# Kernel tuning notes

Hardware: AMD Instinct MI355X
Metric: run time of the kernel (lower is better)

Reference implementation:

```python
import jax, jax.numpy as jnp
import numpy as np

CX = 256  # args.Cx in the original repo (hidden channel dim)

def setup_inputs() -> dict:
    key = jax.random.key(0)
    kK, kV, kQ = jax.random.split(key, 3)
    N, Cx, Tx, Ty = 16, CX, 2048, 2048
    K = jax.random.normal(kK, (N, Cx, Tx), dtype=jnp.float32)
    V = jax.random.normal(kV, (N, Cx, Tx), dtype=jnp.float32)
    Q = jax.random.normal(kQ, (N, Cx, Ty), dtype=jnp.float32)
    return {"K": K, "V": V, "Q": Q}

def reference(K, V, Q):
    # scores: (N, Tx, Ty) = K^T Q / sqrt(Cx)
    scale = 1.0 / np.sqrt(CX).astype(np.float32)
    scores = jnp.einsum('nct,ncy->nty', K, Q) * scale
    A = jax.nn.softmax(scores, axis=1)          # softmax over Tx (dim=1)
    R = jnp.einsum('nct,nty->ncy', V, A)         # (N, Cx, Ty)
    return (R, A)
```

## Files before the change

### kernel.cpp

```cpp
#include <hip/hip_runtime.h>

#define NB 16
#define CX 256
#define TX 2048
#define TY 2048
#define SCALE 0.0625f

typedef __attribute__((ext_vector_type(8))) short short8;
typedef __attribute__((ext_vector_type(4))) short short4v;
typedef __attribute__((ext_vector_type(4))) float floatx4;

__device__ float L_dev[NB * TY];

static __device__ __forceinline__ short f2bf(float x) {
#if defined(__gfx950__)
    __bf16 b = (__bf16)x;
    return __builtin_bit_cast(short, b);
#else
    union { float f; unsigned u; } v; v.f = x;
    unsigned r = v.u + 0x7fff + ((v.u >> 16) & 1);
    return (short)(r >> 16);
#endif
}

__global__ __launch_bounds__(256) void k_prep(const float* __restrict__ K,
                                              const float* __restrict__ Q,
                                              short* __restrict__ KT,
                                              short* __restrict__ QT) {
    __shared__ float Tsh[32][36];
    const int tid = threadIdx.x;
    const int t0  = blockIdx.x * 32;
    const int c0  = blockIdx.y * 32;
    const int isQ = blockIdx.z & 1;
    const int n   = blockIdx.z >> 1;
    const float* src = (isQ ? Q : K) + (size_t)n * CX * TX;
    short*       dst = (isQ ? QT : KT) + (size_t)n * TX * CX;
    const float scale = isQ ? 1.0f : SCALE;

    const int r  = tid >> 3;
    const int q4 = (tid & 7) * 4;
    *(floatx4*)&Tsh[r][q4] =
        *(const floatx4*)(src + (size_t)(c0 + r) * TX + t0 + q4);
    __syncthreads();
    short4v o = { f2bf(Tsh[q4 + 0][r] * scale),
                  f2bf(Tsh[q4 + 1][r] * scale),
                  f2bf(Tsh[q4 + 2][r] * scale),
                  f2bf(Tsh[q4 + 3][r] * scale) };
    *(short4v*)(dst + (size_t)(t0 + r) * CX + c0 + q4) = o;
}

__global__ __launch_bounds__(256) void k_zero() {
    L_dev[blockIdx.x * 256 + threadIdx.x] = 0.f;
}

__global__ __launch_bounds__(256) void k_scores2(const short* __restrict__ KT,
                                                 const short* __restrict__ QT,
                                                 float* __restrict__ S) {
    __shared__ short Ksh[128][40];
    __shared__ short Qsh[128][40];
    __shared__ float Lsh[128];
    const int tid = threadIdx.x;
    const int n  = blockIdx.z;
    const int t0 = blockIdx.y * 128;
    const int y0 = blockIdx.x * 128;

    const short* Ka = KT + ((size_t)n * TX + t0) * CX;
    const short* Qa = QT + ((size_t)n * TY + y0) * CX;

    if (tid < 128) Lsh[tid] = 0.f;

    const int sr = tid >> 1;
    const int sc = (tid & 1) * 16;
    const short* Kp = Ka + (size_t)sr * CX + sc;
    const short* Qp = Qa + (size_t)sr * CX + sc;

    const int lane = tid & 63;
    const int w    = tid >> 6;
    const int wy   = (w >> 1) * 64;
    const int wt   = (w & 1) * 64;
    const int fr   = lane & 15;
    const int fq   = lane >> 4;

    floatx4 acc[4][4];
#pragma unroll
    for (int i = 0; i < 4; ++i)
#pragma unroll
        for (int j = 0; j < 4; ++j) acc[i][j] = (floatx4)0.f;

    short8 ra0 = *(const short8*)(Kp + 0);
    short8 ra1 = *(const short8*)(Kp + 8);
    short8 rb0 = *(const short8*)(Qp + 0);
    short8 rb1 = *(const short8*)(Qp + 8);

    for (int k0 = 0; k0 < CX; k0 += 32) {
        *(short8*)&Ksh[sr][sc]     = ra0;
        *(short8*)&Ksh[sr][sc + 8] = ra1;
        *(short8*)&Qsh[sr][sc]     = rb0;
        *(short8*)&Qsh[sr][sc + 8] = rb1;
        __syncthreads();
        if (k0 + 32 < CX) {
            ra0 = *(const short8*)(Kp + k0 + 32);
            ra1 = *(const short8*)(Kp + k0 + 40);
            rb0 = *(const short8*)(Qp + k0 + 32);
            rb1 = *(const short8*)(Qp + k0 + 40);
        }
        short8 af[4], bv[4];
#pragma unroll
        for (int mt = 0; mt < 4; ++mt)
            af[mt] = *(short8*)&Qsh[wy + mt * 16 + fr][fq * 8];
#pragma unroll
        for (int nt = 0; nt < 4; ++nt)
            bv[nt] = *(short8*)&Ksh[wt + nt * 16 + fr][fq * 8];
#pragma unroll
        for (int mt = 0; mt < 4; ++mt)
#pragma unroll
            for (int nt = 0; nt < 4; ++nt)
                acc[mt][nt] = __builtin_amdgcn_mfma_f32_16x16x32_bf16(
                    af[mt], bv[nt], acc[mt][nt], 0, 0, 0);
        __syncthreads();
    }

    float* Sp = S + (size_t)n * TX * TY;
#pragma unroll
    for (int nt = 0; nt < 4; ++nt) {
        const size_t trow = (size_t)(t0 + wt + nt * 16 + fr) * TY;
#pragma unroll
        for (int mt = 0; mt < 4; ++mt)
            *(floatx4*)&Sp[trow + y0 + wy + mt * 16 + fq * 4] = acc[mt][nt];
    }

#pragma unroll
    for (int mt = 0; mt < 4; ++mt) {
#pragma unroll
        for (int reg = 0; reg < 4; ++reg) {
            float v = 0.f;
#pragma unroll
            for (int nt = 0; nt < 4; ++nt) v += __expf(acc[mt][nt][reg]);
            v += __shfl_xor(v, 1);
            v += __shfl_xor(v, 2);
            v += __shfl_xor(v, 4);
            v += __shfl_xor(v, 8);
            if (fr == 0) atomicAdd(&Lsh[wy + mt * 16 + fq * 4 + reg], v);
        }
    }
    __syncthreads();
    if (tid < 128) atomicAdd(&L_dev[(size_t)n * TY + y0 + tid], Lsh[tid]);
}

__global__ __launch_bounds__(512) void k_pv2(const float* __restrict__ V,
                                             float* __restrict__ SA,
                                             float* __restrict__ R) {
    __shared__ short Vsh[256][40];
    __shared__ short Psh[128][40];
    const int tid = threadIdx.x;
    const int n  = blockIdx.y;
    const int y0 = blockIdx.x * 128;

    const float* Vp = V + (size_t)n * CX * TX;
    float* Ap = SA + (size_t)n * TX * TY + y0;
    float* Rp = R + (size_t)n * CX * TY;

    const int tt = tid & 7;
    const int tc = tid >> 3;
    const int sy = tid & 127;
    const int kh = tid >> 7;

    const float inv = 1.0f / L_dev[(size_t)n * TY + y0 + sy];

    const int lane = tid & 63;
    const int w    = tid >> 6;
    const int wy   = (w & 1) * 64;
    const int wc   = (w >> 1) * 64;
    const int fr   = lane & 15;
    const int fq   = lane >> 4;

    floatx4 acc[4][4];
#pragma unroll
    for (int i = 0; i < 4; ++i)
#pragma unroll
        for (int j = 0; j < 4; ++j) acc[i][j] = (floatx4)0.f;

    for (int k0 = 0; k0 < TX; k0 += 32) {
#pragma unroll
        for (int cc = 0; cc < 4; ++cc) {
            const int c = cc * 64 + tc;
            floatx4 v = *(const floatx4*)(Vp + (size_t)c * TX + k0 + tt * 4);
            short4v sv = {f2bf(v[0]), f2bf(v[1]), f2bf(v[2]), f2bf(v[3])};
            *(short4v*)&Vsh[c][tt * 4] = sv;
        }
#pragma unroll
        for (int g = 0; g < 2; ++g) {
            const int t = k0 + kh * 8 + g * 4;
            float* a0p = Ap + (size_t)(t + 0) * TY + sy;
            float* a1p = Ap + (size_t)(t + 1) * TY + sy;
            float* a2p = Ap + (size_t)(t + 2) * TY + sy;
            float* a3p = Ap + (size_t)(t + 3) * TY + sy;
            float a0 = __expf(*a0p) * inv;
            float a1 = __expf(*a1p) * inv;
            float a2 = __expf(*a2p) * inv;
            float a3 = __expf(*a3p) * inv;
            *a0p = a0; *a1p = a1; *a2p = a2; *a3p = a3;
            short4v pv = {f2bf(a0), f2bf(a1), f2bf(a2), f2bf(a3)};
            *(short4v*)&Psh[sy][kh * 8 + g * 4] = pv;
        }
        __syncthreads();
        short8 af[4], bv[4];
#pragma unroll
        for (int mt = 0; mt < 4; ++mt)
            af[mt] = *(short8*)&Psh[wy + mt * 16 + fr][fq * 8];
#pragma unroll
        for (int nt = 0; nt < 4; ++nt)
            bv[nt] = *(short8*)&Vsh[wc + nt * 16 + fr][fq * 8];
#pragma unroll
        for (int mt = 0; mt < 4; ++mt)
#pragma unroll
            for (int nt = 0; nt < 4; ++nt)
                acc[mt][nt] = __builtin_amdgcn_mfma_f32_16x16x32_bf16(
                    af[mt], bv[nt], acc[mt][nt], 0, 0, 0);
        __syncthreads();
    }

#pragma unroll
    for (int nt = 0; nt < 4; ++nt) {
        const size_t crow = (size_t)(wc + nt * 16 + fr) * TY;
#pragma unroll
        for (int mt = 0; mt < 4; ++mt)
            *(floatx4*)&Rp[crow + y0 + wy + mt * 16 + fq * 4] = acc[mt][nt];
    }
}

extern "C" void kernel_launch(void* const* d_in, const int* in_sizes, int n_in,
                              void* d_out, int out_size, void* d_ws, size_t ws_size,
                              hipStream_t stream) {
    (void)in_sizes; (void)n_in; (void)out_size; (void)d_ws; (void)ws_size;
    const float* K = (const float*)d_in[0];
    const float* V = (const float*)d_in[1];
    const float* Q = (const float*)d_in[2];
    float* R = (float*)d_out;
    float* A = (float*)d_out + (size_t)NB * CX * TY;
    short* KT = (short*)d_out;
    short* QT = KT + (size_t)NB * TX * CX;

    dim3 blk(256);
    k_prep   <<<dim3(TX / 32, CX / 32, NB * 2), blk, 0, stream>>>(K, Q, KT, QT);
    k_zero   <<<dim3(NB * TY / 256), blk, 0, stream>>>();
    k_scores2<<<dim3(TY / 128, TX / 128, NB), blk, 0, stream>>>(KT, QT, A);
    k_pv2    <<<dim3(TY / 128, NB), dim3(512), 0, stream>>>(V, A, R);
}
```

Before: 608.1 us.

## Store exponentials in scores kernel and register-prefetch V and A in PV kernel

The scores kernel now writes exp(score) instead of the raw score, so the PV kernel only multiplies by the inverse row sum instead of recomputing exp. The PV kernel is restructured to 256 threads over 64-column y tiles, which gives twice as many blocks. It also prefetches the next V tile and A values into registers so global loads overlap with the MFMA work. This raises register pressure, and V is re-read and converted once per y tile, so more blocks means more total V traffic.

```diff
diff --git a/kernel.cpp b/kernel.cpp
--- a/kernel.cpp
+++ b/kernel.cpp
@@ -55,7 +55,7 @@
 
 __global__ __launch_bounds__(256) void k_scores2(const short* __restrict__ KT,
                                                  const short* __restrict__ QT,
-                                                 float* __restrict__ S) {
+                                                 float* __restrict__ E) {
     __shared__ short Ksh[128][40];
     __shared__ short Qsh[128][40];
     __shared__ float Lsh[128];
@@ -120,13 +120,18 @@
         __syncthreads();
     }
 
-    float* Sp = S + (size_t)n * TX * TY;
+    float* Ep = E + (size_t)n * TX * TY;
 #pragma unroll
     for (int nt = 0; nt < 4; ++nt) {
         const size_t trow = (size_t)(t0 + wt + nt * 16 + fr) * TY;
 #pragma unroll
-        for (int mt = 0; mt < 4; ++mt)
-            *(floatx4*)&Sp[trow + y0 + wy + mt * 16 + fq * 4] = acc[mt][nt];
+        for (int mt = 0; mt < 4; ++mt) {
+            floatx4 e;
+#pragma unroll
+            for (int c = 0; c < 4; ++c) e[c] = __expf(acc[mt][nt][c]);
+            acc[mt][nt] = e;
+            *(floatx4*)&Ep[trow + y0 + wy + mt * 16 + fq * 4] = e;
+        }
     }
 
 #pragma unroll
@@ -135,7 +140,7 @@
         for (int reg = 0; reg < 4; ++reg) {
             float v = 0.f;
 #pragma unroll
-            for (int nt = 0; nt < 4; ++nt) v += __expf(acc[mt][nt][reg]);
+            for (int nt = 0; nt < 4; ++nt) v += acc[mt][nt][reg];
             v += __shfl_xor(v, 1);
             v += __shfl_xor(v, 2);
             v += __shfl_xor(v, 4);
@@ -147,30 +152,29 @@
     if (tid < 128) atomicAdd(&L_dev[(size_t)n * TY + y0 + tid], Lsh[tid]);
 }
 
-__global__ __launch_bounds__(512) void k_pv2(const float* __restrict__ V,
-                                             float* __restrict__ SA,
+__global__ __launch_bounds__(256) void k_pv3(const float* __restrict__ V,
+                                             float* __restrict__ EA,
                                              float* __restrict__ R) {
     __shared__ short Vsh[256][40];
-    __shared__ short Psh[128][40];
+    __shared__ short Psh[64][40];
     const int tid = threadIdx.x;
     const int n  = blockIdx.y;
-    const int y0 = blockIdx.x * 128;
+    const int y0 = blockIdx.x * 64;
 
     const float* Vp = V + (size_t)n * CX * TX;
-    float* Ap = SA + (size_t)n * TX * TY + y0;
+    float* Ap = EA + (size_t)n * TX * TY + y0;
     float* Rp = R + (size_t)n * CX * TY;
 
     const int tt = tid & 7;
     const int tc = tid >> 3;
-    const int sy = tid & 127;
-    const int kh = tid >> 7;
+    const int sy = tid & 63;
+    const int kh = tid >> 6;
 
     const float inv = 1.0f / L_dev[(size_t)n * TY + y0 + sy];
 
     const int lane = tid & 63;
     const int w    = tid >> 6;
-    const int wy   = (w & 1) * 64;
-    const int wc   = (w >> 1) * 64;
+    const int wc   = w * 64;
     const int fr   = lane & 15;
     const int fq   = lane >> 4;
 
@@ -180,34 +184,46 @@
 #pragma unroll
         for (int j = 0; j < 4; ++j) acc[i][j] = (floatx4)0.f;
 
+    floatx4 rv[8];
+    float   ra[8];
+#pragma unroll
+    for (int cc = 0; cc < 8; ++cc)
+        rv[cc] = *(const floatx4*)(Vp + (size_t)(cc * 32 + tc) * TX + tt * 4);
+#pragma unroll
+    for (int j = 0; j < 8; ++j)
+        ra[j] = Ap[(size_t)(kh * 8 + j) * TY + sy];
+
     for (int k0 = 0; k0 < TX; k0 += 32) {
-#pragma unroll
-        for (int cc = 0; cc < 4; ++cc) {
-            const int c = cc * 64 + tc;
-            floatx4 v = *(const floatx4*)(Vp + (size_t)c * TX + k0 + tt * 4);
-            short4v sv = {f2bf(v[0]), f2bf(v[1]), f2bf(v[2]), f2bf(v[3])};
-            *(short4v*)&Vsh[c][tt * 4] = sv;
-        }
-#pragma unroll
-        for (int g = 0; g < 2; ++g) {
-            const int t = k0 + kh * 8 + g * 4;
-            float* a0p = Ap + (size_t)(t + 0) * TY + sy;
-            float* a1p = Ap + (size_t)(t + 1) * TY + sy;
-            float* a2p = Ap + (size_t)(t + 2) * TY + sy;
-            float* a3p = Ap + (size_t)(t + 3) * TY + sy;
-            float a0 = __expf(*a0p) * inv;
-            float a1 = __expf(*a1p) * inv;
-            float a2 = __expf(*a2p) * inv;
-            float a3 = __expf(*a3p) * inv;
-            *a0p = a0; *a1p = a1; *a2p = a2; *a3p = a3;
-            short4v pv = {f2bf(a0), f2bf(a1), f2bf(a2), f2bf(a3)};
-            *(short4v*)&Psh[sy][kh * 8 + g * 4] = pv;
-        }
-        __syncthreads();
+        float a[8];
+#pragma unroll
+        for (int j = 0; j < 8; ++j) a[j] = ra[j] * inv;
+#pragma unroll
+        for (int j = 0; j < 8; ++j)
+            Ap[(size_t)(k0 + kh * 8 + j) * TY + sy] = a[j];
+        short8 ps = { f2bf(a[0]), f2bf(a[1]), f2bf(a[2]), f2bf(a[3]),
+                      f2bf(a[4]), f2bf(a[5]), f2bf(a[6]), f2bf(a[7]) };
+        *(short8*)&Psh[sy][kh * 8] = ps;
+#pragma unroll
+        for (int cc = 0; cc < 8; ++cc) {
+            short4v sv = {f2bf(rv[cc][0]), f2bf(rv[cc][1]),
+                          f2bf(rv[cc][2]), f2bf(rv[cc][3])};
+            *(short4v*)&Vsh[cc * 32 + tc][tt * 4] = sv;
+        }
+        __syncthreads();
+        if (k0 + 32 < TX) {
+            const int k1 = k0 + 32;
+#pragma unroll
+            for (int cc = 0; cc < 8; ++cc)
+                rv[cc] = *(const floatx4*)(Vp + (size_t)(cc * 32 + tc) * TX +
+                                           k1 + tt * 4);
+#pragma unroll
+            for (int j = 0; j < 8; ++j)
+                ra[j] = Ap[(size_t)(k1 + kh * 8 + j) * TY + sy];
+        }
         short8 af[4], bv[4];
 #pragma unroll
         for (int mt = 0; mt < 4; ++mt)
-            af[mt] = *(short8*)&Psh[wy + mt * 16 + fr][fq * 8];
+            af[mt] = *(short8*)&Psh[mt * 16 + fr][fq * 8];
 #pragma unroll
         for (int nt = 0; nt < 4; ++nt)
             bv[nt] = *(short8*)&Vsh[wc + nt * 16 + fr][fq * 8];
@@ -225,7 +241,7 @@
         const size_t crow = (size_t)(wc + nt * 16 + fr) * TY;
 #pragma unroll
         for (int mt = 0; mt < 4; ++mt)
-            *(floatx4*)&Rp[crow + y0 + wy + mt * 16 + fq * 4] = acc[mt][nt];
+            *(floatx4*)&Rp[crow + y0 + mt * 16 + fq * 4] = acc[mt][nt];
     }
 }
 
@@ -245,5 +261,5 @@
     k_prep   <<<dim3(TX / 32, CX / 32, NB * 2), blk, 0, stream>>>(K, Q, KT, QT);
     k_zero   <<<dim3(NB * TY / 256), blk, 0, stream>>>();
     k_scores2<<<dim3(TY / 128, TX / 128, NB), blk, 0, stream>>>(KT, QT, A);
-    k_pv2    <<<dim3(TY / 128, NB), dim3(512), 0, stream>>>(V, A, R);
-}
+    k_pv3    <<<dim3(TY / 64, NB), blk, 0, stream>>>(V, A, R);
+}
```

Result: faster. 590.7 us (-2.9%).
